# Performance work log

Hardware: AMD Instinct MI355X
Metric: run time of the kernel (lower is better)

Reference implementation:

```python
import jax, jax.numpy as jnp
import numpy as np
import math

# ---- config (matches SSD init) ----
NUM_CLASSES = 8
PRE_NMS_TOPK = 200
NMS_THR = 0.45
DET_PER_IMG = 200
LOW_SCORE = 0.01
BBOX_W = (10.0, 10.0, 5.0, 5.0)
FEAT = [128, 64, 32, 16, 8, 4]
ARS = [[2], [2, 3], [2, 3], [2, 3], [2], [2]]
SCALES = [0.07, 0.15, 0.33, 0.51, 0.69, 0.87, 1.0]
BATCH = 32


def _make_default_boxes():
    # exact math of generate_default_boxes (xyxy, normalized coords)
    out = []
    for k, (f, ars) in enumerate(zip(FEAT, ARS)):
        sp = math.sqrt(SCALES[k] * SCALES[k + 1])
        wh = [[sp, sp]] + [[SCALES[k] * math.sqrt(a), SCALES[k] / math.sqrt(a)] for a in ars]
        wh = np.asarray(wh, np.float32)            # [n,2]
        s = ((np.arange(f) + 0.5) / f).astype(np.float32)
        gy, gx = np.meshgrid(s, s, indexing='ij')
        c = np.stack([gx.ravel(), gy.ravel()], -1)  # [HW,2], y-major
        n = wh.shape[0]
        c = np.repeat(c, n, axis=0)                 # per-loc n copies
        w = np.tile(wh, (f * f, 1))
        out.append(np.concatenate([c, w], 1))
    b = np.concatenate(out, 0)
    return np.concatenate([b[:, :2] - 0.5 * b[:, 2:], b[:, :2] + 0.5 * b[:, 2:]], 1)


def setup_inputs() -> dict:
    key = jax.random.key(0)
    k1, k2 = jax.random.split(key)
    dbox = jnp.asarray(_make_default_boxes())          # [A,4]
    A = dbox.shape[0]
    cls_logits = jax.random.normal(k1, (BATCH, A, NUM_CLASSES), jnp.float32)
    bbox_deltas = jax.random.normal(k2, (BATCH, A, 4), jnp.float32)
    return {"cls_logits": cls_logits, "bbox_deltas": bbox_deltas, "default_boxes": dbox}


def _decode(deltas, dbox):
    # apply_deltas: [B,A,4] deltas, [A,4] xyxy default boxes -> [B,A,4] xyxy
    w = dbox[:, 2] - dbox[:, 0]
    h = dbox[:, 3] - dbox[:, 1]
    cx = dbox[:, 0] + 0.5 * w
    cy = dbox[:, 1] + 0.5 * h
    pcx = deltas[..., 0] / BBOX_W[0] * w + cx
    pcy = deltas[..., 1] / BBOX_W[1] * h + cy
    pw = jnp.exp(deltas[..., 2] / BBOX_W[2]) * w
    ph = jnp.exp(deltas[..., 3] / BBOX_W[3]) * h
    return jnp.stack([pcx - 0.5 * pw, pcy - 0.5 * ph, pcx + 0.5 * pw, pcy + 0.5 * ph], -1)


def _nms_single(boxes, scores, labels):
    # boxes [M,4], scores [M], labels [M] int32; class-aware (batched) NMS
    M = scores.shape[0]
    s = jnp.where(scores > LOW_SCORE, scores, -jnp.inf)
    obox = boxes + labels.astype(boxes.dtype)[:, None] * 4.0  # class offset (boxes in [0,1])
    s_ng = jax.lax.stop_gradient(s)
    ob_all = jax.lax.stop_gradient(obox)
    order = jnp.argsort(-s_ng)
    ob = ob_all[order]
    area = (ob[:, 2] - ob[:, 0]) * (ob[:, 3] - ob[:, 1])
    idx = jnp.arange(M)
    keep0 = jnp.isfinite(s_ng[order])

    def body(keep, i):
        xl = jnp.maximum(ob[i, 0], ob[:, 0])
        yt = jnp.maximum(ob[i, 1], ob[:, 1])
        xr = jnp.minimum(ob[i, 2], ob[:, 2])
        yb = jnp.minimum(ob[i, 3], ob[:, 3])
        inter = jnp.clip(xr - xl, 0.0) * jnp.clip(yb - yt, 0.0)
        iou = inter / (area[i] + area - inter)
        sup = (iou > NMS_THR) & (idx > i) & keep[i]
        return keep & ~sup, None

    keep, _ = jax.lax.scan(body, keep0, idx)
    final = jnp.where(keep, s_ng[order], -jnp.inf)
    top_s, top_i = jax.lax.top_k(final, DET_PER_IMG)
    sel = order[top_i]
    m = jnp.isfinite(top_s)
    out_boxes = jnp.where(m[:, None], boxes[sel], 0.0)
    out_scores = jnp.where(m, scores[sel], 0.0)
    out_labels = jnp.where(m, labels[sel], 0)
    return out_boxes, out_scores, out_labels


def reference(cls_logits, bbox_deltas, default_boxes):
    B, A, C = cls_logits.shape
    scores = jax.nn.softmax(cls_logits, axis=-1)               # [B,A,C]
    boxes = jnp.clip(_decode(bbox_deltas, default_boxes), 0.0, 1.0)  # [B,A,4]
    fg = jnp.swapaxes(scores[..., 1:], 1, 2)                   # [B,C-1,A]
    top_v, top_i = jax.lax.top_k(fg, PRE_NMS_TOPK)             # [B,C-1,K]
    bsel = jnp.take_along_axis(boxes[:, None], top_i[..., None], axis=2)  # [B,C-1,K,4]
    labels = jnp.broadcast_to(jnp.arange(1, C, dtype=jnp.int32)[:, None], (C - 1, PRE_NMS_TOPK))
    M = (C - 1) * PRE_NMS_TOPK
    sf = top_v.reshape(B, M)
    bf = bsel.reshape(B, M, 4)
    lf = labels.reshape(M)
    return jax.vmap(_nms_single, in_axes=(0, 0, None))(bf, sf, lf)
```

## Files before the change

### kernel.cpp

```cpp
#include <hip/hip_runtime.h>
#include <hip/hip_bf16.h>
#include <math.h>


#define NCLS 8
#define NFG 7
#define TOPK 200
#define NMSM (NFG * TOPK)
#define HSLICE 24
#define LOW_SCORE 0.01f
#define NMS_THR 0.45f
#define BINS 2048
#define HREP 4
#define CAP 4096

__global__ __launch_bounds__(1024) void score_kernel(
    const float* __restrict__ logits, unsigned* __restrict__ skeys32, int A) {
  int tid = threadIdx.x;
  int b = blockIdx.y;
  int slice = blockIdx.x;
  int sl = A / HSLICE;
  int a0 = slice * sl;
  int npair = sl >> 1;
  if (tid >= npair) return;
  int a = a0 + 2 * tid;
  const float4* p4 = (const float4*)(logits + ((size_t)b * A + a) * NCLS);
  float4 v0 = p4[0], v1 = p4[1], v2 = p4[2], v3 = p4[3];
  float x0[NCLS] = {v0.x, v0.y, v0.z, v0.w, v1.x, v1.y, v1.z, v1.w};
  float x1[NCLS] = {v2.x, v2.y, v2.z, v2.w, v3.x, v3.y, v3.z, v3.w};
  float mx0 = x0[0], mx1 = x1[0];
#pragma unroll
  for (int c = 1; c < NCLS; c++) { mx0 = fmaxf(mx0, x0[c]); mx1 = fmaxf(mx1, x1[c]); }
  float e0[NCLS], e1[NCLS];
  float s0 = 0.0f, s1 = 0.0f;
#pragma unroll
  for (int c = 0; c < NCLS; c++) {
    e0[c] = expf(x0[c] - mx0); s0 += e0[c];
    e1[c] = expf(x1[c] - mx1); s1 += e1[c];
  }
  float i0 = 1.0f / s0, i1 = 1.0f / s1;
#pragma unroll
  for (int c = 1; c < NCLS; c++) {
    unsigned k0 = __float_as_uint(e0[c] * i0) >> 16;
    unsigned k1 = __float_as_uint(e1[c] * i1) >> 16;
    skeys32[(((size_t)b * NFG + (c - 1)) * A + a) >> 1] = k0 | (k1 << 16);
  }
}

__global__ __launch_bounds__(1024) void select_kernel(
    const unsigned short* __restrict__ skeys, const float* __restrict__ logits,
    int A, float* __restrict__ tval, int* __restrict__ tidx) {
  __shared__ unsigned hist[HREP * BINS];
  __shared__ unsigned buf[CAP];
  __shared__ unsigned long long fin[CAP];
  __shared__ unsigned fineh[8];
  __shared__ int s_t, s_above, s_thr, s_cnt, s_cnt2;
  int tid = threadIdx.x;
  int row = blockIdx.x;
  int b = row / NFG;
  int cc = row - b * NFG;
  if (tid == 0) { s_cnt = 0; s_cnt2 = 0; }
  if (tid < 8) fineh[tid] = 0u;
  for (int i = tid; i < HREP * BINS; i += 1024) hist[i] = 0u;
  __syncthreads();

  unsigned* myh = hist + (tid & (HREP - 1)) * BINS;
  const uint4* p4 = (const uint4*)(skeys + (size_t)row * A);
  int n8 = A / 8;
  for (int k = tid; k < n8; k += 1024) {
    uint4 v = p4[k];
    unsigned wds[4] = {v.x, v.y, v.z, v.w};
#pragma unroll
    for (int w = 0; w < 4; w++) {
      atomicAdd(&myh[(wds[w] & 0xFFFFu) >> 3], 1u);
      atomicAdd(&myh[(wds[w] >> 19)], 1u);
    }
  }
  __syncthreads();

  if (tid < 64) {
    int lane = tid;
    int s = 0;
#pragma unroll
    for (int r = 0; r < HREP; r++) {
      const uint4* h4 = (const uint4*)(hist + r * BINS);
#pragma unroll
      for (int k = 0; k < 8; k++) {
        uint4 v = h4[lane * 8 + k];
        s += (int)(v.x + v.y + v.z + v.w);
      }
    }
    int sfx = s;
#pragma unroll
    for (int off = 1; off < 64; off <<= 1) {
      int o = __shfl(sfx, lane + off);
      sfx += (lane + off < 64) ? o : 0;
    }
    int nxt = __shfl(sfx, lane + 1);
    nxt = (lane < 63) ? nxt : 0;
    bool mine = (sfx >= TOPK) && (nxt < TOPK);
    if (mine) {
      int cum = nxt;
      int t = lane * 32 + 31;
      for (; t >= lane * 32; t--) {
        int hb = (int)(hist[t] + hist[BINS + t] + hist[2 * BINS + t] +
                       hist[3 * BINS + t]);
        cum += hb;
        if (cum >= TOPK) { s_above = cum - hb; break; }
      }
      s_t = t;
    }
  }
  __syncthreads();

  unsigned tbin = (unsigned)s_t;
  for (int k = tid; k < n8; k += 1024) {
    uint4 v = p4[k];
    unsigned wds[4] = {v.x, v.y, v.z, v.w};
#pragma unroll
    for (int w = 0; w < 4; w++) {
#pragma unroll
      for (int hf = 0; hf < 2; hf++) {
        unsigned k16 = (wds[w] >> (16 * hf)) & 0xFFFFu;
        if ((k16 >> 3) >= tbin) {
          int pos = atomicAdd(&s_cnt, 1);
          if (pos < CAP) buf[pos] = (k16 << 16) | (unsigned)(8 * k + 2 * w + hf);
          if ((k16 >> 3) == tbin) atomicAdd(&fineh[k16 & 7u], 1u);
        }
      }
    }
  }
  __syncthreads();

  if (tid == 0) {
    int need = TOPK - s_above;
    int sfx = 0, t2 = 0;
    for (int t = 7; t >= 0; t--) {
      sfx += (int)fineh[t];
      if (sfx >= need) { t2 = t; break; }
    }
    s_thr = (int)((tbin << 3) | (unsigned)t2);
  }
  __syncthreads();

  unsigned thr = (unsigned)s_thr;
  int cnt = s_cnt; if (cnt > CAP) cnt = CAP;
  for (int i = tid; i < cnt; i += 1024) {
    unsigned v = buf[i];
    if ((v >> 16) >= thr) {
      int idx = (int)(v & 0xFFFFu);
      const float4* lp = (const float4*)(logits + ((size_t)b * A + idx) * NCLS);
      float4 v0 = lp[0], v1 = lp[1];
      float x[NCLS] = {v0.x, v0.y, v0.z, v0.w, v1.x, v1.y, v1.z, v1.w};
      float mx = x[0];
#pragma unroll
      for (int c = 1; c < NCLS; c++) mx = fmaxf(mx, x[c]);
      float e[NCLS];
      float s = 0.0f;
#pragma unroll
      for (int c = 0; c < NCLS; c++) { e[c] = expf(x[c] - mx); s += e[c]; }
      float inv = 1.0f / s;
      unsigned bits = __float_as_uint(e[cc + 1] * inv);
      int p = atomicAdd(&s_cnt2, 1);
      if (p < CAP)
        fin[p] = ((unsigned long long)bits << 32) | (unsigned)(~idx);
    }
  }
  __syncthreads();
  int cnt2 = s_cnt2; if (cnt2 > CAP) cnt2 = CAP;
  size_t obase = (size_t)row * TOPK;

  for (int i = tid; i < cnt2; i += 1024) {
    unsigned long long my = fin[i];
    int r = 0;
    for (int j = 0; j < cnt2; j++) r += (fin[j] > my);
    if (r < TOPK) {
      tval[obase + r] = __uint_as_float((unsigned)(my >> 32));
      tidx[obase + r] = (int)(~(unsigned)(my & 0xFFFFFFFFull));
    }
  }
  for (int r = cnt2 + tid; r < TOPK; r += 1024) {
    tval[obase + r] = 0.0f;
    tidx[obase + r] = 0;
  }
}

__global__ __launch_bounds__(256) void nms_class_kernel(
    const float* __restrict__ deltas, const float* __restrict__ dbox,
    const float* __restrict__ tval, const int* __restrict__ tidx,
    unsigned long long* __restrict__ gskeep, int A) {
  __shared__ float bx0[200], by0[200], bx1[200], by1[200], bar_[200];
  __shared__ unsigned long long smask[256][4];
  __shared__ int s_nv;
  int tid = threadIdx.x;
  int row = blockIdx.x;
  int b = row / NFG;
  int cc = row - b * NFG;
  if (tid == 0) s_nv = 0;
  __syncthreads();

  float off = 4.0f * (float)(cc + 1);
  if (tid < 200) {
    size_t tk = (size_t)row * TOPK + tid;
    int a = tidx[tk];
    if (a < 0) a = 0;
    float v = tval[tk];
    const float* db = dbox + (size_t)a * 4;
    float w = db[2] - db[0];
    float h = db[3] - db[1];
    float cx = db[0] + 0.5f * w;
    float cy = db[1] + 0.5f * h;
    const float* dd = deltas + ((size_t)b * A + a) * 4;
    float pcx = dd[0] / 10.0f * w + cx;
    float pcy = dd[1] / 10.0f * h + cy;
    float pw = expf(dd[2] / 5.0f) * w;
    float ph = expf(dd[3] / 5.0f) * h;
    float x0 = fminf(fmaxf(pcx - 0.5f * pw, 0.0f), 1.0f);
    float y0 = fminf(fmaxf(pcy - 0.5f * ph, 0.0f), 1.0f);
    float x1 = fminf(fmaxf(pcx + 0.5f * pw, 0.0f), 1.0f);
    float y1 = fminf(fmaxf(pcy + 0.5f * ph, 0.0f), 1.0f);
    float sx0 = x0 + off, sy0 = y0 + off, sx1 = x1 + off, sy1 = y1 + off;
    bx0[tid] = sx0; by0[tid] = sy0; bx1[tid] = sx1; by1[tid] = sy1;
    bar_[tid] = (sx1 - sx0) * (sy1 - sy0);
    if (v > LOW_SCORE) atomicAdd(&s_nv, 1);
  }
  __syncthreads();

  {
    unsigned long long w0 = 0ull, w1 = 0ull, w2 = 0ull, w3 = 0ull;
    int i = tid;
    if (i < 200) {
      float x0 = bx0[i], y0 = by0[i], x1 = bx1[i], y1 = by1[i], a = bar_[i];
#pragma unroll 4
      for (int j = 0; j < 200; j++) {
        float xl = fmaxf(x0, bx0[j]);
        float yt = fmaxf(y0, by0[j]);
        float xr = fminf(x1, bx1[j]);
        float yb = fminf(y1, by1[j]);
        float inter = fmaxf(xr - xl, 0.0f) * fmaxf(yb - yt, 0.0f);
        float iou = inter / (a + bar_[j] - inter);
        if (j > i && iou > NMS_THR) {
          unsigned long long bit = 1ull << (j & 63);
          int wsel = j >> 6;
          if (wsel == 0) w0 |= bit;
          else if (wsel == 1) w1 |= bit;
          else if (wsel == 2) w2 |= bit;
          else w3 |= bit;
        }
      }
    }
    smask[tid][0] = w0; smask[tid][1] = w1;
    smask[tid][2] = w2; smask[tid][3] = w3;
  }
  __syncthreads();

  int nv = s_nv;
  if (tid < 64) {
    int lane = tid;
    bool act = (lane < 4);
    int li = act ? lane : 0;
    unsigned long long remove = 0ull;
    if (act) {
      int base = lane * 64;
      if (base + 64 <= nv) remove = ~0ull;
      else if (base < nv) remove = (~0ull) >> (64 - (nv - base));
    }
#pragma unroll
    for (int bi = 0; bi < 4; bi++) {
      unsigned long long cur = __shfl(remove, bi);
      unsigned long long wmask = (act && lane >= bi) ? ~0ull : 0ull;
#pragma unroll 8
      for (int d = 0; d < 64; d++) {
        int i = bi * 64 + d;
        unsigned long long rowd  = smask[i][li];
        unsigned long long diagd = smask[i][bi];
        bool kd = (cur >> d) & 1ull;
        cur    &= ~(kd ? diagd : 0ull);
        remove &= ~(kd ? (rowd & wmask) : 0ull);
      }
      remove = (lane == bi) ? cur : remove;
    }
    if (act) gskeep[(size_t)row * 4 + lane] = remove;
  }
}

__global__ __launch_bounds__(1024) void nms_merge_kernel(
    const float* __restrict__ deltas, const float* __restrict__ dbox,
    const float* __restrict__ tval, const int* __restrict__ tidx,
    const unsigned long long* __restrict__ gskeep,
    float* __restrict__ out, int A, int B) {
  __shared__ unsigned long long keys[NMSM];
  __shared__ unsigned long long keep[NFG][4];
  int tid = threadIdx.x;
  int b = blockIdx.x;
  if (tid < NFG * 4) keep[tid >> 2][tid & 3] = gskeep[(size_t)b * NFG * 4 + tid];
  for (int m = tid; m < NMSM; m += 1024) {
    float v = tval[(size_t)b * NMSM + m];
    keys[m] = ((unsigned long long)__float_as_uint(v) << 32) | (unsigned)(~m);
  }
  __syncthreads();

  float* ob = out + (size_t)b * TOPK * 4;
  float* os = out + (size_t)B * TOPK * 4 + (size_t)b * TOPK;
  float* ol = out + (size_t)B * TOPK * 5 + (size_t)b * TOPK;
  for (int r = tid; r < TOPK; r += 1024) {
    ob[r * 4 + 0] = 0.0f; ob[r * 4 + 1] = 0.0f;
    ob[r * 4 + 2] = 0.0f; ob[r * 4 + 3] = 0.0f;
    os[r] = 0.0f; ol[r] = 0.0f;
  }
  __syncthreads();

  for (int m = tid; m < NMSM; m += 1024) {
    int cc = m / TOPK;
    int r = m - cc * TOPK;
    if (!((keep[cc][r >> 6] >> (r & 63)) & 1ull)) continue;
    unsigned long long k = keys[m];
    int lo[NFG], hi[NFG];
#pragma unroll
    for (int c2 = 0; c2 < NFG; c2++) { lo[c2] = 0; hi[c2] = TOPK; }
#pragma unroll
    for (int s8 = 0; s8 < 8; s8++) {
#pragma unroll
      for (int c2 = 0; c2 < NFG; c2++) {
        if (lo[c2] < hi[c2]) {
          int mid = (lo[c2] + hi[c2]) >> 1;
          if (keys[c2 * TOPK + mid] > k) lo[c2] = mid + 1; else hi[c2] = mid;
        }
      }
    }
    int rank = 0;
#pragma unroll
    for (int c2 = 0; c2 < NFG; c2++) {
      int l = lo[c2];
#pragma unroll
      for (int w = 0; w < 4; w++) {
        int base = w * 64;
        if (l >= base + 64) rank += (int)__popcll(keep[c2][w]);
        else if (l > base)
          rank += (int)__popcll(keep[c2][w] & ((1ull << (l - base)) - 1ull));
      }
    }
    if (rank < TOPK) {
      size_t tk = (size_t)b * NMSM + m;
      int a = tidx[tk];
      if (a < 0) a = 0;
      float v = tval[tk];
      const float* db = dbox + (size_t)a * 4;
      float w = db[2] - db[0];
      float h = db[3] - db[1];
      float cx = db[0] + 0.5f * w;
      float cy = db[1] + 0.5f * h;
      const float* dd = deltas + ((size_t)b * A + a) * 4;
      float pcx = dd[0] / 10.0f * w + cx;
      float pcy = dd[1] / 10.0f * h + cy;
      float pw = expf(dd[2] / 5.0f) * w;
      float ph = expf(dd[3] / 5.0f) * h;
      float x0 = fminf(fmaxf(pcx - 0.5f * pw, 0.0f), 1.0f);
      float y0 = fminf(fmaxf(pcy - 0.5f * ph, 0.0f), 1.0f);
      float x1 = fminf(fmaxf(pcx + 0.5f * pw, 0.0f), 1.0f);
      float y1 = fminf(fmaxf(pcy + 0.5f * ph, 0.0f), 1.0f);
      ob[rank * 4 + 0] = x0; ob[rank * 4 + 1] = y0;
      ob[rank * 4 + 2] = x1; ob[rank * 4 + 3] = y1;
      os[rank] = v;
      ol[rank] = (float)(cc + 1);
    }
  }
}

extern "C" void kernel_launch(void* const* d_in, const int* in_sizes, int n_in,
                              void* d_out, int out_size, void* d_ws, size_t ws_size,
                              hipStream_t stream) {
  const float* logits = (const float*)d_in[0];
  const float* deltas = (const float*)d_in[1];
  const float* dbox   = (const float*)d_in[2];
  int A = in_sizes[2] / 4;
  int B = in_sizes[0] / (A * NCLS);
  int NROWS = B * NFG;
  float* out = (float*)d_out;

  unsigned short* skeys = (unsigned short*)d_ws;
  float* tval = (float*)(skeys + (size_t)B * NFG * A);
  int*   tidx = (int*)(tval + (size_t)B * NFG * TOPK);
  unsigned long long* gskeep =
      (unsigned long long*)(tidx + (size_t)B * NFG * TOPK);

  score_kernel<<<dim3(HSLICE, B), 1024, 0, stream>>>(logits, (unsigned*)skeys, A);
  select_kernel<<<NROWS, 1024, 0, stream>>>(skeys, logits, A, tval, tidx);
  nms_class_kernel<<<NROWS, 256, 0, stream>>>(deltas, dbox, tval, tidx,
                                              gskeep, A);
  nms_merge_kernel<<<B, 1024, 0, stream>>>(deltas, dbox, tval, tidx, gskeep,
                                           out, A, B);
}
```

Measured before the change: 91.53 us.

## Fuse per-class NMS mask into select kernel and split IoU rows across four threads

```diff
diff --git a/kernel.cpp b/kernel.cpp
--- a/kernel.cpp
+++ b/kernel.cpp
@@ -49,17 +49,23 @@
 
 __global__ __launch_bounds__(1024) void select_kernel(
     const unsigned short* __restrict__ skeys, const float* __restrict__ logits,
-    int A, float* __restrict__ tval, int* __restrict__ tidx) {
+    const float* __restrict__ deltas, const float* __restrict__ dbox,
+    int A, float* __restrict__ tval, int* __restrict__ tidx,
+    unsigned long long* __restrict__ gskeep) {
   __shared__ unsigned hist[HREP * BINS];
   __shared__ unsigned buf[CAP];
   __shared__ unsigned long long fin[CAP];
   __shared__ unsigned fineh[8];
-  __shared__ int s_t, s_above, s_thr, s_cnt, s_cnt2;
+  __shared__ float rtval[TOPK];
+  __shared__ int rtidx[TOPK];
+  __shared__ float rbx0[TOPK], rby0[TOPK], rbx1[TOPK], rby1[TOPK], rbar[TOPK];
+  __shared__ unsigned long long smask[256][4];
+  __shared__ int s_t, s_above, s_thr, s_cnt, s_cnt2, s_nv;
   int tid = threadIdx.x;
   int row = blockIdx.x;
   int b = row / NFG;
   int cc = row - b * NFG;
-  if (tid == 0) { s_cnt = 0; s_cnt2 = 0; }
+  if (tid == 0) { s_cnt = 0; s_cnt2 = 0; s_nv = 0; }
   if (tid < 8) fineh[tid] = 0u;
   for (int i = tid; i < HREP * BINS; i += 1024) hist[i] = 0u;
   __syncthreads();
@@ -141,6 +147,7 @@
     }
     s_thr = (int)((tbin << 3) | (unsigned)t2);
   }
+  if (tid < TOPK) { rtval[tid] = 0.0f; rtidx[tid] = 0; }
   __syncthreads();
 
   unsigned thr = (unsigned)s_thr;
@@ -175,36 +182,23 @@
     int r = 0;
     for (int j = 0; j < cnt2; j++) r += (fin[j] > my);
     if (r < TOPK) {
-      tval[obase + r] = __uint_as_float((unsigned)(my >> 32));
-      tidx[obase + r] = (int)(~(unsigned)(my & 0xFFFFFFFFull));
+      float fv = __uint_as_float((unsigned)(my >> 32));
+      int fi = (int)(~(unsigned)(my & 0xFFFFFFFFull));
+      tval[obase + r] = fv;  rtval[r] = fv;
+      tidx[obase + r] = fi;  rtidx[r] = fi;
     }
   }
   for (int r = cnt2 + tid; r < TOPK; r += 1024) {
     tval[obase + r] = 0.0f;
     tidx[obase + r] = 0;
   }
-}
-
-__global__ __launch_bounds__(256) void nms_class_kernel(
-    const float* __restrict__ deltas, const float* __restrict__ dbox,
-    const float* __restrict__ tval, const int* __restrict__ tidx,
-    unsigned long long* __restrict__ gskeep, int A) {
-  __shared__ float bx0[200], by0[200], bx1[200], by1[200], bar_[200];
-  __shared__ unsigned long long smask[256][4];
-  __shared__ int s_nv;
-  int tid = threadIdx.x;
-  int row = blockIdx.x;
-  int b = row / NFG;
-  int cc = row - b * NFG;
-  if (tid == 0) s_nv = 0;
-  __syncthreads();
-
-  float off = 4.0f * (float)(cc + 1);
-  if (tid < 200) {
-    size_t tk = (size_t)row * TOPK + tid;
-    int a = tidx[tk];
+  __syncthreads();
+
+  float offc = 4.0f * (float)(cc + 1);
+  if (tid < TOPK) {
+    int a = rtidx[tid];
     if (a < 0) a = 0;
-    float v = tval[tk];
+    float v = rtval[tid];
     const float* db = dbox + (size_t)a * 4;
     float w = db[2] - db[0];
     float h = db[3] - db[1];
@@ -219,38 +213,36 @@
     float y0 = fminf(fmaxf(pcy - 0.5f * ph, 0.0f), 1.0f);
     float x1 = fminf(fmaxf(pcx + 0.5f * pw, 0.0f), 1.0f);
     float y1 = fminf(fmaxf(pcy + 0.5f * ph, 0.0f), 1.0f);
-    float sx0 = x0 + off, sy0 = y0 + off, sx1 = x1 + off, sy1 = y1 + off;
-    bx0[tid] = sx0; by0[tid] = sy0; bx1[tid] = sx1; by1[tid] = sy1;
-    bar_[tid] = (sx1 - sx0) * (sy1 - sy0);
+    float sx0 = x0 + offc, sy0 = y0 + offc, sx1 = x1 + offc, sy1 = y1 + offc;
+    rbx0[tid] = sx0; rby0[tid] = sy0; rbx1[tid] = sx1; rby1[tid] = sy1;
+    rbar[tid] = (sx1 - sx0) * (sy1 - sy0);
     if (v > LOW_SCORE) atomicAdd(&s_nv, 1);
   }
   __syncthreads();
 
   {
-    unsigned long long w0 = 0ull, w1 = 0ull, w2 = 0ull, w3 = 0ull;
-    int i = tid;
-    if (i < 200) {
-      float x0 = bx0[i], y0 = by0[i], x1 = bx1[i], y1 = by1[i], a = bar_[i];
-#pragma unroll 4
-      for (int j = 0; j < 200; j++) {
-        float xl = fmaxf(x0, bx0[j]);
-        float yt = fmaxf(y0, by0[j]);
-        float xr = fminf(x1, bx1[j]);
-        float yb = fminf(y1, by1[j]);
-        float inter = fmaxf(xr - xl, 0.0f) * fmaxf(yb - yt, 0.0f);
-        float iou = inter / (a + bar_[j] - inter);
-        if (j > i && iou > NMS_THR) {
-          unsigned long long bit = 1ull << (j & 63);
-          int wsel = j >> 6;
-          if (wsel == 0) w0 |= bit;
-          else if (wsel == 1) w1 |= bit;
-          else if (wsel == 2) w2 |= bit;
-          else w3 |= bit;
+    int i = tid >> 2;
+    int w = tid & 3;
+    unsigned long long bits = 0ull;
+    if (i < TOPK && 64 * w + 63 > i) {
+      float x0 = rbx0[i], y0 = rby0[i], x1 = rbx1[i], y1 = rby1[i];
+      float a = rbar[i];
+      int j0 = 64 * w;
+#pragma unroll 8
+      for (int d = 0; d < 64; d++) {
+        int j = j0 + d;
+        if (j < TOPK) {
+          float xl = fmaxf(x0, rbx0[j]);
+          float yt = fmaxf(y0, rby0[j]);
+          float xr = fminf(x1, rbx1[j]);
+          float yb = fminf(y1, rby1[j]);
+          float inter = fmaxf(xr - xl, 0.0f) * fmaxf(yb - yt, 0.0f);
+          float iou = inter / (a + rbar[j] - inter);
+          if (j > i && iou > NMS_THR) bits |= 1ull << d;
         }
       }
     }
-    smask[tid][0] = w0; smask[tid][1] = w1;
-    smask[tid][2] = w2; smask[tid][3] = w3;
+    smask[i][w] = bits;
   }
   __syncthreads();
 
@@ -385,9 +377,8 @@
       (unsigned long long*)(tidx + (size_t)B * NFG * TOPK);
 
   score_kernel<<<dim3(HSLICE, B), 1024, 0, stream>>>(logits, (unsigned*)skeys, A);
-  select_kernel<<<NROWS, 1024, 0, stream>>>(skeys, logits, A, tval, tidx);
-  nms_class_kernel<<<NROWS, 256, 0, stream>>>(deltas, dbox, tval, tidx,
-                                              gskeep, A);
+  select_kernel<<<NROWS, 1024, 0, stream>>>(skeys, logits, deltas, dbox, A,
+                                            tval, tidx, gskeep);
   nms_merge_kernel<<<B, 1024, 0, stream>>>(deltas, dbox, tval, tidx, gskeep,
                                            out, A, B);
 }
```

Result: faster. 77.71 us (-15.1%).
